# Kernel optimization log

Measured on AMD Instinct MI355X. Metric: run time of the kernel, lower is better.

## Reference

```python
import jax, jax.numpy as jnp
import numpy as np

N_OBJS = 100          # max detections / scatter buffer size
TOP_K = 100           # top_k_n peaks per channel
KP_THRES = 0.3        # score threshold before NMS
NMS_IOU = 0.5
RESIZE_H, RESIZE_W = 1536.0, 1536.0   # resize_shape (== heatmap HxW here)
H, W = 1536, 1536


def _peak_hms(hms):
    # 3x3 stride-1 SAME max pool; keep only local maxima (Base.apply_max_pool)
    hmax = jax.lax.reduce_window(hms, -jnp.inf, jax.lax.max, (1, 3, 3, 1), (1, 1, 1, 1), 'SAME')
    return jnp.where(hms == hmax, hms, 0.0)


def _top_k_loc(hms, k):
    # per-channel top-k peak coordinates -> [b, c, k, 2] (y, x) int32
    b, h, w, c = hms.shape
    flat = jnp.transpose(hms, (0, 3, 1, 2)).reshape(b, c, h * w)
    _, idx = jax.lax.top_k(flat, k)
    return jnp.stack([idx // w, idx % w], axis=-1).astype(jnp.int32)


def _iou_matrix(boxes):
    # boxes [N,4] = (y1,x1,y2,x2)
    y1, x1, y2, x2 = boxes[:, 0], boxes[:, 1], boxes[:, 2], boxes[:, 3]
    area = jnp.maximum(y2 - y1, 0.0) * jnp.maximum(x2 - x1, 0.0)
    iy1 = jnp.maximum(y1[:, None], y1[None, :]); ix1 = jnp.maximum(x1[:, None], x1[None, :])
    iy2 = jnp.minimum(y2[:, None], y2[None, :]); ix2 = jnp.minimum(x2[:, None], x2[None, :])
    inter = jnp.maximum(iy2 - iy1, 0.0) * jnp.maximum(ix2 - ix1, 0.0)
    union = area[:, None] + area[None, :] - inter
    return inter / jnp.maximum(union, 1e-8)


def _nms_single(boxes, scores):
    # greedy single-class NMS, fixed-size (combined_non_max_suppression equivalent,
    # clip_boxes=False, score_threshold=-inf); padded slots are zeros like TF.
    order = jnp.argsort(-scores)
    boxes, scores = boxes[order], scores[order]
    n = boxes.shape[0]
    iou = _iou_matrix(boxes)
    idxs = jnp.arange(n)

    def step(suppressed, inp):
        i, iou_row = inp
        keep_i = ~suppressed[i]
        return suppressed | (keep_i & (iou_row > NMS_IOU) & (idxs > i)), keep_i

    _, keep = jax.lax.scan(step, jnp.zeros(n, bool), (idxs, iou))
    perm = jnp.argsort(jnp.where(keep, 0, 1))  # stable: compact kept to front, score order preserved
    keep_s = keep[perm]
    out_boxes = jnp.where(keep_s[:, None], boxes[perm], 0.0)
    out_scores = jnp.where(keep_s, scores[perm], 0.0)
    return out_boxes, out_scores, jnp.zeros(n, jnp.float32)


def _forward(obj_heat_map, offset_map, size_maps, origin_shapes):
    resize_shape = jnp.array([RESIZE_H, RESIZE_W], jnp.float32)
    ratio = origin_shapes / resize_shape                      # [b,2]
    hms = _peak_hms(obj_heat_map)                             # [b,H,W,2]
    b = hms.shape[0]
    coors = _top_k_loc(hms, TOP_K)                            # [b,2,K,2]
    b_coors, b_lnmks = coors[:, :1], coors[:, 1:]             # obj / nose coords
    bidx = jnp.arange(b)[:, None, None]

    # nose landmark: scores at nose-channel peaks, masked mean of coords (int mean like TF)
    nose_scores = hms[bidx, b_lnmks[..., 0], b_lnmks[..., 1], 1]     # [b,1,K]
    nose_mask = nose_scores > 0.5
    cnt = jnp.maximum(jnp.sum(nose_mask), 1)
    lnmk_mean = jnp.sum(jnp.where(nose_mask[..., None], b_lnmks, 0), axis=(0, 1, 2)) // cnt
    b_lnmks_m = lnmk_mean.reshape(b, 1, 2)                    # requires b == 1 (as in original)
    b_nose_scores = jnp.where(nose_mask, nose_scores, -1.0).reshape(b, -1)

    # boxes from sizes at object peaks
    size_vals = size_maps[bidx, b_coors[..., 0], b_coors[..., 1]]    # [b,1,K,2]
    obj_scores = hms[bidx, b_coors[..., 0], b_coors[..., 1], 0]      # [b,1,K]
    centers = b_coors.astype(jnp.float32)
    tls = jnp.maximum(centers - size_vals / 2.0, 0.0)
    brs = jnp.minimum(centers + size_vals / 2.0, resize_shape - 1.0)
    bboxes = jnp.concatenate([tls, brs], axis=-1) * jnp.tile(ratio, (1, 2))[:, None, None, :]
    bboxes, scores = bboxes[:, 0], obj_scores[:, 0]           # [b,K,4], [b,K]

    # scatter masked candidates into -1-initialized buffer (tensor_scatter_nd_update equivalent)
    mask = scores > KP_THRES
    cand = jnp.where(mask[..., None], jnp.concatenate([bboxes, scores[..., None]], -1), -1.0)
    cand = jnp.pad(cand, ((0, 0), (0, N_OBJS - TOP_K), (0, 0)), constant_values=-1.0)  # [b,N_OBJS,5]

    nb, ns, nc = jax.vmap(_nms_single)(cand[..., :4], cand[..., 4])
    box_results = jnp.where(nb == -1.0, jnp.inf, nb)
    box_results = jnp.where(box_results == 0.0, jnp.inf, box_results)  # (x - 1 == -1)
    b_bboxes = jnp.concatenate([box_results, ns[..., None], nc[..., None]], axis=-1)  # [b,N_OBJS,6]

    # offset vectors at the mean nose landmark (gather 8ch -> [b,n,4,2])
    bidx2 = jnp.arange(b)[:, None]
    off = offset_map[bidx2, b_lnmks_m[..., 0], b_lnmks_m[..., 1]].reshape(b, 1, 4, 2)
    lf = b_lnmks_m.astype(jnp.float32)
    b_ENM = (lf[:, :, None, :] - off) * ratio[:, None, None, :]
    b_lnmks_out = lf * ratio[:, None, :]
    return b_bboxes, b_lnmks_out, b_ENM, b_nose_scores


def setup_inputs() -> dict:
    key = jax.random.key(0)
    k1, k2, k3 = jax.random.split(key, 3)
    obj_heat_map = jax.random.uniform(k1, (1, H, W, 2), jnp.float32)
    offset_map = jax.random.normal(k2, (1, H, W, 8), jnp.float32) * 8.0
    size_maps = jax.random.uniform(k3, (1, H, W, 2), jnp.float32) * 128.0
    origin_shapes = jnp.array([[1080.0, 1920.0]], jnp.float32)
    return {"obj_heat_map": obj_heat_map, "offset_map": offset_map,
            "size_maps": size_maps, "origin_shapes": origin_shapes}


def reference(obj_heat_map, offset_map, size_maps, origin_shapes):
    return _forward(obj_heat_map, offset_map, size_maps, origin_shapes)
```

## Files before the change

kernel.cpp:

```cpp
#include <hip/hip_runtime.h>
#include <cstdint>

#define IW 1536
#define IH 1536
#define TOPK 100
#define CAPP 327680
#define CAPB 128
#define CAPT 8192
#define BF_INF16 0x7F7Fu

typedef unsigned u32; typedef unsigned long long u64; typedef unsigned short u16;

#define OH1   0
#define OCNT  4096
#define OSEL  4102
#define OLSD  4106
#define OZEND 4172
#define OPK   4172
#define OPV   (OPK + 2*CAPP)
#define OLB   (OPV + CAPP)
#define OLT   (OLB + 4*CAPB)

__device__ __forceinline__ u32 enc16(u32 b){ b &= 0xFFFFu; return (b & 0x8000u) ? ((~b)&0xFFFFu) : (b|0x8000u); }
__device__ __forceinline__ u32 dec16(u32 e){ return (e & 0x8000u) ? (e^0x8000u) : ((~e)&0xFFFFu); }
__device__ __forceinline__ float up16(u32 b){ return __uint_as_float((b&0xFFFFu)<<16); }
__device__ __forceinline__ u16 f2bf(float f){ u32 u=__float_as_uint(f); return (u16)((u + 0x7FFFu + ((u>>16)&1u))>>16); }

__device__ __forceinline__ void wave_sel2048(const u32* bins, u32 need, int* Dout, u32* Aout){
  int lane = threadIdx.x & 63;
  u32 s = 0;
  #pragma unroll
  for(int k=0;k<32;++k) s += bins[lane*32+k];
  u32 c = s;
  #pragma unroll
  for(int off=1;off<64;off<<=1){
    u32 v = __shfl_down(c, off, 64);
    if(lane + off < 64) c += v;
  }
  u32 cnext = __shfl_down(c, 1, 64); if(lane==63) cnext = 0u;
  u64 m = __ballot(c >= need);
  if(m == 0ull){ if(lane==0){ *Dout = 0; *Aout = 0u; } return; }
  int L = 63 - __builtin_clzll((unsigned long long)m);
  if(lane == L){
    u32 above = cnext; int D = 32*L;
    for(int b=32*L+31; b>=32*L; --b){
      u32 h = bins[b];
      if(above + h >= need){ D = b; break; }
      above += h;
    }
    *Dout = D; *Aout = above;
  }
}

__global__ __launch_bounds__(1024) void scan_kernel(const u32* __restrict__ hm, u32* __restrict__ ws){
  __shared__ u32 lh[4096];
  __shared__ u32 lbuf[2][1600];
  __shared__ u16 vbuf[2][1600];
  __shared__ u32 lcnt[2], lbase[2];
  int tid = threadIdx.x, lane = tid & 63;
  for(int i=tid;i<4096;i+=1024) lh[i]=0u;
  if(tid<2) lcnt[tid]=0u;
  __syncthreads();

  int p = (blockIdx.x*1024 + tid)*4;
  int y = p / IW, x = p - y*IW;
  const u32* R1 = hm + y*IW;
  const u32* R0 = y ? R1 - IW : R1;
  const u32* R2 = (y < IH-1) ? R1 + IW : R1;
  uint4 c0 = *(const uint4*)(R0+x), c1 = *(const uint4*)(R1+x), c2 = *(const uint4*)(R2+x);
  int xl = x ? x-1 : 0, xr = (x+4 < IW) ? x+4 : IW-1;
  u32 a0[6] = {R0[xl], c0.x, c0.y, c0.z, c0.w, R0[xr]};
  u32 a1[6] = {R1[xl], c1.x, c1.y, c1.z, c1.w, R1[xr]};
  u32 a2[6] = {R2[xl], c2.x, c2.y, c2.z, c2.w, R2[xr]};

  #pragma unroll
  for(int j=0;j<4;++j){
    u32 cc = a1[j+1];
    u32 cl = cc & 0xFFFFu, chv = cc >> 16;
    u32 m0=0u, m1=0u;
    #pragma unroll
    for(int d=0;d<3;++d){
      u32 n0=a0[j+d], n2=a2[j+d]; u32 t;
      t=n0&0xFFFFu; m0=t>m0?t:m0;  t=n0>>16; m1=t>m1?t:m1;
      t=n2&0xFFFFu; m0=t>m0?t:m0;  t=n2>>16; m1=t>m1?t:m1;
    }
    { u32 n=a1[j];   u32 t=n&0xFFFFu; m0=t>m0?t:m0; t=n>>16; m1=t>m1?t:m1; }
    { u32 n=a1[j+2]; u32 t=n&0xFFFFu; m0=t>m0?t:m0; t=n>>16; m1=t>m1?t:m1; }
    bool pk0 = (cl >= m0), pk1 = (chv >= m1);
    u32 idx = (u32)(p + j);

    u64 mk0 = __ballot(pk0);
    if(mk0){
      u32 cw = __popcll(mk0), b;
      if(lane==0) b = atomicAdd(&lcnt[0], cw);
      b = __shfl(b, 0);
      if(pk0){
        u32 pos = b + __popcll(mk0 & ((1ull<<lane)-1ull));
        if(pos < 1600){ lbuf[0][pos] = idx; vbuf[0][pos] = (u16)cl; }
      }
    }
    u64 mk1 = __ballot(pk1);
    if(mk1){
      u32 cw = __popcll(mk1), b;
      if(lane==0) b = atomicAdd(&lcnt[1], cw);
      b = __shfl(b, 0);
      if(pk1){
        u32 pos = b + __popcll(mk1 & ((1ull<<lane)-1ull));
        if(pos < 1600){ lbuf[1][pos] = idx; vbuf[1][pos] = (u16)chv; }
      }
    }
    if(pk0) atomicAdd(&lh[enc16(cl)>>5], 1u);
    if(pk1) atomicAdd(&lh[2048 + (enc16(chv)>>5)], 1u);
  }
  __syncthreads();
  if(tid < 2){
    u32 n = lcnt[tid]; if(n > 1600) n = 1600;
    lcnt[tid] = n;
    lbase[tid] = atomicAdd(&ws[OCNT+tid], n);
  }
  __syncthreads();
  u16* pv = (u16*)(ws + OPV);
  for(int ch=0;ch<2;++ch){
    u32 n = lcnt[ch], base = lbase[ch];
    for(u32 i=tid;i<n;i+=1024){
      u32 g = base + i;
      if(g < CAPP){ ws[OPK + ch*CAPP + g] = lbuf[ch][i]; pv[ch*CAPP + g] = vbuf[ch][i]; }
    }
  }
  for(int i=tid;i<4096;i+=1024) if(lh[i]) atomicAdd(&ws[OH1+i], lh[i]);
}

#define GRID2 128
__global__ __launch_bounds__(1024) void mid_kernel(u32* __restrict__ ws){
  __shared__ u32 lhh[4096];
  __shared__ u64 tbuf[2][2048];
  __shared__ u32 tcnt[2], tbase[2];
  __shared__ u32 lsdl[64];
  __shared__ int Dsh[2]; __shared__ u32 Ash[2];
  int tid = threadIdx.x, lane = tid & 63;
  for(int i=tid;i<4096;i+=1024) lhh[i] = ws[OH1+i];
  if(tid < 2) tcnt[tid] = 0u;
  if(tid < 64) lsdl[tid] = 0u;
  __syncthreads();
  if(tid < 64)       wave_sel2048(lhh,        (u32)TOPK, &Dsh[0], &Ash[0]);
  else if(tid < 128) wave_sel2048(lhh + 2048, (u32)TOPK, &Dsh[1], &Ash[1]);
  __syncthreads();
  if(blockIdx.x == 0 && tid < 2){ ws[OSEL+tid] = (u32)Dsh[tid]; ws[OSEL+2+tid] = Ash[tid]; }

  const u16* pv = (const u16*)(ws + OPV);
  u64* listB = (u64*)(ws + OLB);
  for(int ch=0;ch<2;++ch){
    u32 n = ws[OCNT+ch]; if(n > CAPP) n = CAPP;
    int D = Dsh[ch];
    for(u32 base = blockIdx.x*1024; base < n; base += GRID2*1024){
      u32 i = base + tid;
      bool act = (i < n);
      u32 e = 0, idx = 0;
      if(act){ e = enc16(pv[ch*CAPP + i]); idx = ws[OPK + ch*CAPP + i]; }
      if(act && (int)(e>>5) > D){
        u32 pos = atomicAdd(&ws[OCNT+2+ch], 1u);
        if(pos < CAPB) listB[ch*CAPB + pos] = ((u64)e<<32) | (u32)(~idx);
      }
      bool isT = act && ((int)(e>>5) == D);
      if(isT) atomicAdd(&lsdl[ch*32 + (e & 31u)], 1u);
      u64 mk = __ballot(isT);
      if(mk){
        u32 cw = __popcll(mk), b;
        if(lane==0) b = atomicAdd(&tcnt[ch], cw);
        b = __shfl(b, 0);
        if(isT){
          u32 pos = b + __popcll(mk & ((1ull<<lane)-1ull));
          if(pos < 2048) tbuf[ch][pos] = ((u64)e<<32) | (u32)(~idx);
        }
      }
    }
  }
  __syncthreads();
  if(tid < 2){
    u32 c = tcnt[tid]; if(c > 2048) c = 2048;
    tcnt[tid] = c;
    tbase[tid] = atomicAdd(&ws[OCNT+4+tid], c);
  }
  __syncthreads();
  u64* tie = (u64*)(ws + OLT);
  for(int ch=0;ch<2;++ch)
    for(u32 i=tid;i<tcnt[ch];i+=1024){
      u32 g = tbase[ch] + i;
      if(g < CAPT) tie[ch*CAPT + g] = tbuf[ch][i];
    }
  if(tid < 64 && lsdl[tid]) atomicAdd(&ws[OLSD + tid], lsdl[tid]);
}

__global__ __launch_bounds__(256) void finalize_kernel(
    u32* __restrict__ ws, const u32* __restrict__ szm, const u16* __restrict__ offm,
    const u16* __restrict__ orig, u16* __restrict__ out){
  __shared__ u64 tl[CAPT];
  __shared__ u64 keys[CAPB];
  __shared__ u32 h2[2048];
  __shared__ u32 wbits[64];
  __shared__ u32 sel[CAPB];
  __shared__ int Bv, selc, selc2, Lsh;
  __shared__ float oval[TOPK]; __shared__ int oidx[TOPK];
  __shared__ float nval[TOPK]; __shared__ int nidx[TOPK];
  __shared__ float cbox[TOPK][4]; __shared__ float cscore[TOPK]; __shared__ float area[TOPK];
  __shared__ int sup[TOPK]; __shared__ int slotv[TOPK];
  __shared__ u64 nbits[2*TOPK];
  __shared__ u64 suppS[2];
  __shared__ int cS, srS, scS, meanr, meanc;
  int tid = threadIdx.x, lane = tid & 63;

  if(tid < TOPK){ oval[tid]=0.0f; oidx[tid]=0; nval[tid]=0.0f; nidx[tid]=0; }
  __syncthreads();

  for(int ch=0; ch<2; ++ch){
    int nB = (int)ws[OCNT+2+ch]; if(nB > CAPB) nB = CAPB;
    int nT = (int)ws[OCNT+4+ch]; if(nT > CAPT) nT = CAPT;
    int D  = (int)ws[OSEL+ch];
    u32 above = ws[OSEL+2+ch];
    const u64* listB = ((const u64*)(ws + OLB)) + ch*CAPB;
    const u64* tie   = ((const u64*)(ws + OLT)) + ch*CAPT;
    float* dval = ch ? nval : oval;
    int*   didx = ch ? nidx : oidx;

    for(int i=tid;i<nT;i+=256) tl[i] = tie[i];
    for(int i=tid;i<2048;i+=256) h2[i]=0u;
    if(tid < 64) wbits[tid]=0u;
    if(tid == 0){
      selc = 0; selc2 = 0; Bv = 0;
      u32 need2 = (u32)TOPK - above;
      u32 a2 = 0; int L = 0;
      for(int b=31;b>=1;--b){
        u32 h = ws[OLSD + ch*32 + b];
        if(a2 + h >= need2){ L = b; break; }
        a2 += h;
      }
      Lsh = L;
    }
    __syncthreads();
    u32 thr = ((u32)D<<5) | (u32)Lsh;
    float tval = up16(dec16(thr));

    for(int i=tid;i<nB;i+=256){
      int pos = atomicAdd(&selc, 1); if(pos < CAPB) keys[pos] = listB[i];
    }
    for(int i=tid;i<nT;i+=256){
      u64 k = tl[i]; u32 e = (u32)(k>>32);
      if(e > thr){
        int pos = atomicAdd(&selc, 1); if(pos < CAPB) keys[pos] = k;
      } else if(e == thr){
        u32 idx = ~(u32)(k & 0xFFFFFFFFu);
        atomicAdd(&h2[idx>>11], 1u);
      }
    }
    __syncthreads();
    int nA = selc; if(nA > CAPB) nA = CAPB; if(nA > TOPK) nA = TOPK;
    if(tid < nA){
      u64 kreg = keys[tid];
      int r = 0;
      for(int j=0;j<nA;++j) r += (keys[j] > kreg);
      if(r < TOPK){
        dval[r] = up16(dec16((u32)(kreg>>32)));
        didx[r] = (int)(~(u32)(kreg & 0xFFFFFFFFu));
      }
    }
    int need = TOPK - nA;

    if(need > 0){
      if(tid < 64){
        int base = tid*32;
        u32 s = 0;
        #pragma unroll
        for(int k2=0;k2<32;++k2) s += h2[base+k2];
        u32 c = s;
        #pragma unroll
        for(int off=1;off<64;off<<=1){
          u32 v = __shfl_up(c, off, 64);
          if(lane >= off) c += v;
        }
        u64 m = __ballot(c >= (u32)need);
        int L = (int)(__ffsll((unsigned long long)m) - 1);
        if(tid == L){
          u32 cum2 = c - s;
          int B = base;
          for(int k2=0;k2<32;++k2){
            u32 hb = h2[base+k2];
            if(cum2 + hb >= (u32)need){ B = base+k2; break; }
            cum2 += hb;
          }
          Bv = B;
        }
      }
      __syncthreads();
      int B = Bv;
      for(int i=tid;i<nT;i+=256){
        u64 k = tl[i]; u32 e = (u32)(k>>32);
        if(e == thr){
          u32 idx = ~(u32)(k & 0xFFFFFFFFu);
          int b = (int)(idx>>11);
          if(b < B){
            int pos = atomicAdd(&selc2, 1);
            if(pos < CAPB) sel[pos] = idx;
          } else if(b == B){
            atomicOr(&wbits[(idx&2047)>>5], 1u<<(idx&31));
          }
        }
      }
      __syncthreads();
      int sc = selc2; if(sc > CAPB) sc = CAPB;
      if(tid < sc){
        u32 v = sel[tid];
        int r = 0;
        for(int j=0;j<sc;++j) r += (sel[j] < v);
        if(nA + r < TOPK){ dval[nA+r] = tval; didx[nA+r] = (int)v; }
      }
      if(tid == 0){
        int rem = need - sc;
        int pos = nA + sc;
        for(int wi=0; wi<64 && rem>0; ++wi){
          u32 bits = wbits[wi];
          while(bits && rem>0){
            int l = __ffs(bits) - 1;
            bits &= bits - 1;
            if(pos < TOPK){ dval[pos] = tval; didx[pos] = (int)(((u32)Bv<<11) | ((u32)wi<<5) | (u32)l); }
            ++pos; --rem;
          }
        }
      }
    }
    __syncthreads();
  }

  float ry = up16(orig[0]) / 1536.0f;
  float rx = up16(orig[1]) / 1536.0f;

  if(tid == 0){ cS = 0; srS = 0; scS = 0; }
  __syncthreads();
  if(tid < TOPK && nval[tid] > 0.5f){
    atomicAdd(&cS, 1);
    atomicAdd(&srS, nidx[tid] / IW);
    atomicAdd(&scS, nidx[tid] % IW);
  }
  if(tid < TOPK) out[610 + tid] = f2bf(nval[tid] > 0.5f ? nval[tid] : -1.0f);
  __syncthreads();
  if(tid == 0){
    int c = cS < 1 ? 1 : cS;
    meanr = srS / c; meanc = scS / c;
  }

  if(tid < TOPK){
    int idx = oidx[tid];
    int r = idx / IW, c = idx - r*IW;
    float score = oval[tid];
    u32 sz = szm[idx];
    float sy = up16(sz), sx = up16(sz>>16);
    float cy = (float)r, cx = (float)c;
    float tly = fmaxf(cy - sy*0.5f, 0.0f);
    float tlx = fmaxf(cx - sx*0.5f, 0.0f);
    float bry = fminf(cy + sy*0.5f, 1535.0f);
    float brx = fminf(cx + sx*0.5f, 1535.0f);
    bool mk = score > 0.3f;
    float b0 = mk ? tly*ry : -1.0f;
    float b1 = mk ? tlx*rx : -1.0f;
    float b2 = mk ? bry*ry : -1.0f;
    float b3 = mk ? brx*rx : -1.0f;
    cbox[tid][0]=b0; cbox[tid][1]=b1; cbox[tid][2]=b2; cbox[tid][3]=b3;
    cscore[tid] = mk ? score : -1.0f;
    area[tid] = fmaxf(b2-b0,0.0f) * fmaxf(b3-b1,0.0f);
  }
  if(tid < 2*TOPK) nbits[tid] = 0ull;
  __syncthreads();

  for(int t=tid; t<TOPK*TOPK; t+=256){
    int i = t / TOPK, j = t - i*TOPK;
    if(j > i){
      float iy1 = fmaxf(cbox[i][0], cbox[j][0]);
      float ix1 = fmaxf(cbox[i][1], cbox[j][1]);
      float iy2 = fminf(cbox[i][2], cbox[j][2]);
      float ix2 = fminf(cbox[i][3], cbox[j][3]);
      float inter = fmaxf(iy2-iy1,0.0f) * fmaxf(ix2-ix1,0.0f);
      float uni = (area[i] + area[j]) - inter;
      if(inter / fmaxf(uni, 1e-8f) > 0.5f)
        atomicOr(&nbits[i*2 + (j>>6)], 1ull << (j&63));
    }
  }
  __syncthreads();
  if(tid == 0){
    u64 s0 = 0ull, s1 = 0ull;
    for(int i=0;i<TOPK;++i){
      bool su = (i<64) ? ((s0>>i)&1ull) : ((s1>>(i-64))&1ull);
      if(!su){ s0 |= nbits[i*2]; s1 |= nbits[i*2+1]; }
    }
    suppS[0] = s0; suppS[1] = s1;
  }
  __syncthreads();
  if(tid < TOPK) sup[tid] = (int)((suppS[tid>>6] >> (tid&63)) & 1ull);
  __syncthreads();

  if(tid < TOPK){
    int kbefore = 0, sbefore = 0, ktot = 0;
    for(int j=0;j<TOPK;++j){
      int sj = sup[j];
      ktot += (1 - sj);
      if(j < tid){ kbefore += (1 - sj); sbefore += sj; }
    }
    int slot = sup[tid] ? (ktot + sbefore) : kbefore;
    slotv[slot] = tid;
  }
  __syncthreads();

  if(tid < TOPK){
    int s = slotv[tid];
    bool ks = !sup[s];
    u16 row[6];
    if(ks){
      for(int d=0;d<4;++d){
        float v = cbox[s][d];
        row[d] = (v == -1.0f || v == 0.0f) ? (u16)BF_INF16 : f2bf(v);
      }
      row[4] = f2bf(cscore[s]);
    } else {
      for(int d=0;d<4;++d) row[d] = (u16)BF_INF16;
      row[4] = 0;
    }
    row[5] = 0;
    for(int d=0;d<6;++d) out[tid*6 + d] = row[d];
  }

  if(tid == 0){
    float lfy = (float)meanr, lfx = (float)meanc;
    out[600] = f2bf(lfy * ry);
    out[601] = f2bf(lfx * rx);
    const u16* op = offm + ((size_t)meanr*IW + meanc)*8;
    for(int p=0;p<4;++p){
      out[602 + p*2 + 0] = f2bf((lfy - up16(op[p*2+0])) * ry);
      out[602 + p*2 + 1] = f2bf((lfx - up16(op[p*2+1])) * rx);
    }
  }
}

extern "C" void kernel_launch(void* const* d_in, const int* in_sizes, int n_in,
                              void* d_out, int out_size, void* d_ws, size_t ws_size,
                              hipStream_t stream) {
  const u32* heat = (const u32*)d_in[0];
  const u16* offm = (const u16*)d_in[1];
  const u32* szm  = (const u32*)d_in[2];
  const u16* orig = (const u16*)d_in[3];
  u16* out = (u16*)d_out;
  u32* ws = (u32*)d_ws;

  hipMemsetAsync(ws, 0, OZEND*sizeof(u32), stream);
  scan_kernel<<<576, 1024, 0, stream>>>(heat, ws);
  mid_kernel<<<GRID2, 1024, 0, stream>>>(ws);
  finalize_kernel<<<1, 256, 0, stream>>>(ws, szm, offm, orig, out);
}
```

Before: 199.3 us.

## Process both heatmap channels concurrently in finalize kernel with 512 threads

The single-block finalize kernel now runs with 512 threads and assigns one 256-thread half to each channel, so the two channels' top-k selection runs concurrently instead of in a sequential loop. Tie candidates equal to the threshold are compacted into a shared index list on the first pass, so the second pass scans only those instead of re-reading the whole tie list. Header values are preloaded into shared memory. The cost is more shared memory for per-channel buffers and larger blocks, and this only affects the small serial tail kernel.

```diff
diff --git a/kernel.cpp b/kernel.cpp
--- a/kernel.cpp
+++ b/kernel.cpp
@@ -191,15 +191,17 @@
   if(tid < 64 && lsdl[tid]) atomicAdd(&ws[OLSD + tid], lsdl[tid]);
 }
 
-__global__ __launch_bounds__(256) void finalize_kernel(
+__global__ __launch_bounds__(512) void finalize_kernel(
     u32* __restrict__ ws, const u32* __restrict__ szm, const u16* __restrict__ offm,
     const u16* __restrict__ orig, u16* __restrict__ out){
-  __shared__ u64 tl[CAPT];
-  __shared__ u64 keys[CAPB];
-  __shared__ u32 h2[2048];
-  __shared__ u32 wbits[64];
-  __shared__ u32 sel[CAPB];
-  __shared__ int Bv, selc, selc2, Lsh;
+  __shared__ u32 tidxS[2][CAPT];
+  __shared__ u32 h2s[2][2048];
+  __shared__ u64 keysS[2][CAPB];
+  __shared__ u32 selS[2][CAPB];
+  __shared__ u32 wbitsS[2][64];
+  __shared__ u32 lsdS[64];
+  __shared__ u32 hdr[10];
+  __shared__ int selcS[2], selc2S[2], BvS[2], LshS[2], tcS[2];
   __shared__ float oval[TOPK]; __shared__ int oidx[TOPK];
   __shared__ float nval[TOPK]; __shared__ int nidx[TOPK];
   __shared__ float cbox[TOPK][4]; __shared__ float cscore[TOPK]; __shared__ float area[TOPK];
@@ -208,127 +210,130 @@
   __shared__ u64 suppS[2];
   __shared__ int cS, srS, scS, meanr, meanc;
   int tid = threadIdx.x, lane = tid & 63;
-
+  int ch = tid >> 8, ltid = tid & 255;
+
+  if(tid < 10) hdr[tid] = ws[OCNT + tid];
+  if(tid < 64) lsdS[tid] = ws[OLSD + tid];
+  for(int i=tid;i<4096;i+=512) ((u32*)h2s)[i] = 0u;
+  if(tid < 128) ((u32*)wbitsS)[tid] = 0u;
+  if(tid < 4){ selcS[tid&1] = 0; selc2S[tid&1] = 0; }
+  if(tid < 2){ BvS[tid] = 0; LshS[tid] = 0; tcS[tid] = 0; }
   if(tid < TOPK){ oval[tid]=0.0f; oidx[tid]=0; nval[tid]=0.0f; nidx[tid]=0; }
   __syncthreads();
 
-  for(int ch=0; ch<2; ++ch){
-    int nB = (int)ws[OCNT+2+ch]; if(nB > CAPB) nB = CAPB;
-    int nT = (int)ws[OCNT+4+ch]; if(nT > CAPT) nT = CAPT;
-    int D  = (int)ws[OSEL+ch];
-    u32 above = ws[OSEL+2+ch];
-    const u64* listB = ((const u64*)(ws + OLB)) + ch*CAPB;
-    const u64* tie   = ((const u64*)(ws + OLT)) + ch*CAPT;
-    float* dval = ch ? nval : oval;
-    int*   didx = ch ? nidx : oidx;
-
-    for(int i=tid;i<nT;i+=256) tl[i] = tie[i];
-    for(int i=tid;i<2048;i+=256) h2[i]=0u;
-    if(tid < 64) wbits[tid]=0u;
-    if(tid == 0){
-      selc = 0; selc2 = 0; Bv = 0;
-      u32 need2 = (u32)TOPK - above;
-      u32 a2 = 0; int L = 0;
-      for(int b=31;b>=1;--b){
-        u32 h = ws[OLSD + ch*32 + b];
-        if(a2 + h >= need2){ L = b; break; }
-        a2 += h;
-      }
-      Lsh = L;
-    }
-    __syncthreads();
-    u32 thr = ((u32)D<<5) | (u32)Lsh;
-    float tval = up16(dec16(thr));
-
-    for(int i=tid;i<nB;i+=256){
-      int pos = atomicAdd(&selc, 1); if(pos < CAPB) keys[pos] = listB[i];
-    }
-    for(int i=tid;i<nT;i+=256){
-      u64 k = tl[i]; u32 e = (u32)(k>>32);
-      if(e > thr){
-        int pos = atomicAdd(&selc, 1); if(pos < CAPB) keys[pos] = k;
-      } else if(e == thr){
-        u32 idx = ~(u32)(k & 0xFFFFFFFFu);
-        atomicAdd(&h2[idx>>11], 1u);
-      }
-    }
-    __syncthreads();
-    int nA = selc; if(nA > CAPB) nA = CAPB; if(nA > TOPK) nA = TOPK;
-    if(tid < nA){
-      u64 kreg = keys[tid];
-      int r = 0;
-      for(int j=0;j<nA;++j) r += (keys[j] > kreg);
-      if(r < TOPK){
-        dval[r] = up16(dec16((u32)(kreg>>32)));
-        didx[r] = (int)(~(u32)(kreg & 0xFFFFFFFFu));
-      }
-    }
-    int need = TOPK - nA;
-
-    if(need > 0){
-      if(tid < 64){
-        int base = tid*32;
-        u32 s = 0;
-        #pragma unroll
-        for(int k2=0;k2<32;++k2) s += h2[base+k2];
-        u32 c = s;
-        #pragma unroll
-        for(int off=1;off<64;off<<=1){
-          u32 v = __shfl_up(c, off, 64);
-          if(lane >= off) c += v;
-        }
-        u64 m = __ballot(c >= (u32)need);
-        int L = (int)(__ffsll((unsigned long long)m) - 1);
-        if(tid == L){
-          u32 cum2 = c - s;
-          int B = base;
-          for(int k2=0;k2<32;++k2){
-            u32 hb = h2[base+k2];
-            if(cum2 + hb >= (u32)need){ B = base+k2; break; }
-            cum2 += hb;
-          }
-          Bv = B;
-        }
-      }
-      __syncthreads();
-      int B = Bv;
-      for(int i=tid;i<nT;i+=256){
-        u64 k = tl[i]; u32 e = (u32)(k>>32);
-        if(e == thr){
-          u32 idx = ~(u32)(k & 0xFFFFFFFFu);
-          int b = (int)(idx>>11);
-          if(b < B){
-            int pos = atomicAdd(&selc2, 1);
-            if(pos < CAPB) sel[pos] = idx;
-          } else if(b == B){
-            atomicOr(&wbits[(idx&2047)>>5], 1u<<(idx&31));
-          }
-        }
-      }
-      __syncthreads();
-      int sc = selc2; if(sc > CAPB) sc = CAPB;
-      if(tid < sc){
-        u32 v = sel[tid];
-        int r = 0;
-        for(int j=0;j<sc;++j) r += (sel[j] < v);
-        if(nA + r < TOPK){ dval[nA+r] = tval; didx[nA+r] = (int)v; }
-      }
-      if(tid == 0){
-        int rem = need - sc;
-        int pos = nA + sc;
-        for(int wi=0; wi<64 && rem>0; ++wi){
-          u32 bits = wbits[wi];
-          while(bits && rem>0){
-            int l = __ffs(bits) - 1;
-            bits &= bits - 1;
-            if(pos < TOPK){ dval[pos] = tval; didx[pos] = (int)(((u32)Bv<<11) | ((u32)wi<<5) | (u32)l); }
-            ++pos; --rem;
-          }
-        }
-      }
-    }
-    __syncthreads();
-  }
+  int nB = (int)hdr[2+ch]; if(nB > CAPB) nB = CAPB;
+  int nT = (int)hdr[4+ch]; if(nT > CAPT) nT = CAPT;
+  int D  = (int)hdr[6+ch];
+  u32 above = hdr[8+ch];
+  const u64* listB = ((const u64*)(ws + OLB)) + ch*CAPB;
+  const u64* tie   = ((const u64*)(ws + OLT)) + ch*CAPT;
+  float* dval = ch ? nval : oval;
+  int*   didx = ch ? nidx : oidx;
+
+  if(ltid == 0){
+    u32 need2 = (u32)TOPK - above;
+    u32 a2 = 0; int L = 0;
+    for(int b=31;b>=1;--b){
+      u32 h = lsdS[ch*32 + b];
+      if(a2 + h >= need2){ L = b; break; }
+      a2 += h;
+    }
+    LshS[ch] = L;
+    selcS[ch] = nB;
+  }
+  for(int i=ltid;i<nB;i+=256) keysS[ch][i] = listB[i];
+  __syncthreads();
+  u32 thr = ((u32)D<<5) | (u32)LshS[ch];
+  float tval = up16(dec16(thr));
+
+  for(int i=ltid;i<nT;i+=256){
+    u64 k = tie[i]; u32 e = (u32)(k>>32);
+    if(e > thr){
+      int pos = atomicAdd(&selcS[ch], 1); if(pos < CAPB) keysS[ch][pos] = k;
+    } else if(e == thr){
+      u32 idx = ~(u32)(k & 0xFFFFFFFFu);
+      int pos = atomicAdd(&tcS[ch], 1);
+      if(pos < CAPT) tidxS[ch][pos] = idx;
+      atomicAdd(&h2s[ch][idx>>11], 1u);
+    }
+  }
+  __syncthreads();
+
+  int nA = selcS[ch]; if(nA > CAPB) nA = CAPB; if(nA > TOPK) nA = TOPK;
+  int need = TOPK - nA;
+  if(ltid < nA){
+    u64 kreg = keysS[ch][ltid];
+    int r = 0;
+    for(int j=0;j<nA;++j) r += (keysS[ch][j] > kreg);
+    if(r < TOPK){
+      dval[r] = up16(dec16((u32)(kreg>>32)));
+      didx[r] = (int)(~(u32)(kreg & 0xFFFFFFFFu));
+    }
+  }
+  if(ltid < 64){
+    const u32* hh = h2s[ch];
+    int base = lane*32;
+    u32 s = 0;
+    #pragma unroll
+    for(int k2=0;k2<32;++k2) s += hh[base+k2];
+    u32 c = s;
+    #pragma unroll
+    for(int off=1;off<64;off<<=1){
+      u32 v = __shfl_up(c, off, 64);
+      if(lane >= off) c += v;
+    }
+    u64 m = __ballot(need > 0 && c >= (u32)need);
+    int L = m ? (int)(__ffsll((unsigned long long)m) - 1) : -1;
+    if(L >= 0 && lane == L){
+      u32 cum2 = c - s;
+      int B = base;
+      for(int k2=0;k2<32;++k2){
+        u32 hb = hh[base+k2];
+        if(cum2 + hb >= (u32)need){ B = base+k2; break; }
+        cum2 += hb;
+      }
+      BvS[ch] = B;
+    }
+  }
+  __syncthreads();
+
+  int B = BvS[ch];
+  int tc = tcS[ch]; if(tc > CAPT) tc = CAPT;
+  if(need > 0){
+    for(int i=ltid;i<tc;i+=256){
+      u32 idx = tidxS[ch][i];
+      int b = (int)(idx>>11);
+      if(b < B){
+        int pos = atomicAdd(&selc2S[ch], 1);
+        if(pos < CAPB) selS[ch][pos] = idx;
+      } else if(b == B){
+        atomicOr(&wbitsS[ch][(idx&2047)>>5], 1u<<(idx&31));
+      }
+    }
+  }
+  __syncthreads();
+
+  int sc = selc2S[ch]; if(sc > CAPB) sc = CAPB;
+  if(need > 0 && ltid < sc){
+    u32 v = selS[ch][ltid];
+    int r = 0;
+    for(int j=0;j<sc;++j) r += (selS[ch][j] < v);
+    if(nA + r < TOPK){ dval[nA+r] = tval; didx[nA+r] = (int)v; }
+  }
+  if(need > 0 && ltid == 0){
+    int rem = need - sc;
+    int pos = nA + sc;
+    for(int wi=0; wi<64 && rem>0; ++wi){
+      u32 bits = wbitsS[ch][wi];
+      while(bits && rem>0){
+        int l = __ffs(bits) - 1;
+        bits &= bits - 1;
+        if(pos < TOPK){ dval[pos] = tval; didx[pos] = (int)(((u32)B<<11) | ((u32)wi<<5) | (u32)l); }
+        ++pos; --rem;
+      }
+    }
+  }
+  __syncthreads();
 
   float ry = up16(orig[0]) / 1536.0f;
   float rx = up16(orig[1]) / 1536.0f;
@@ -370,7 +375,7 @@
   if(tid < 2*TOPK) nbits[tid] = 0ull;
   __syncthreads();
 
-  for(int t=tid; t<TOPK*TOPK; t+=256){
+  for(int t=tid; t<TOPK*TOPK; t+=512){
     int i = t / TOPK, j = t - i*TOPK;
     if(j > i){
       float iy1 = fmaxf(cbox[i][0], cbox[j][0]);
@@ -451,5 +456,5 @@
   hipMemsetAsync(ws, 0, OZEND*sizeof(u32), stream);
   scan_kernel<<<576, 1024, 0, stream>>>(heat, ws);
   mid_kernel<<<GRID2, 1024, 0, stream>>>(ws);
-  finalize_kernel<<<1, 256, 0, stream>>>(ws, szm, offm, orig, out);
+  finalize_kernel<<<1, 512, 0, stream>>>(ws, szm, offm, orig, out);
 }
```

Result: faster. 185.2 us (-7.1%).
